# Kernel optimization log

Hardware: AMD Instinct MI355X
Metric: run time of the kernel (lower is better)

The kernel has to match this reference:

```python
import jax, jax.numpy as jnp
from jax import lax
import numpy as np

B, C, H, W = 32, 256, 56, 56
G1, G2 = 64, 4          # groups for 3x3 convs, number of parallel convs / 1x1 groups
EPS = 1e-5
DN = ('NCHW', 'OIHW', 'NCHW')


def setup_inputs() -> dict:
    key = jax.random.key(0)
    it = iter(jax.random.split(key, 32))
    nk = lambda: next(it)
    n = lambda shape, s=0.05: jax.random.normal(nk(), shape, jnp.float32) * s
    u = lambda shape: jax.random.uniform(nk(), shape, jnp.float32, minval=0.5, maxval=1.5)
    inp = {'x': jax.random.normal(nk(), (B, C, H, W), jnp.float32)}
    inp.update(
        w1=n((G2, G1, C // G1, 3, 3), 0.1), b1=n((G2, G1)),
        bn1a_g=1.0 + n((C,)), bn1a_b=n((C,)), bn1a_m=n((C,)), bn1a_v=u((C,)),
        pw1=n((C, C // G2, 1, 1), 0.1), pb1=n((C,)),
        bn1b_g=1.0 + n((C,)), bn1b_b=n((C,)), bn1b_m=n((C,)), bn1b_v=u((C,)),
        w2=n((G2, G1, C // G1, 3, 3), 0.1), b2=n((G2, G1)),
        bn2a_g=1.0 + n((C,)), bn2a_b=n((C,)), bn2a_m=n((C,)), bn2a_v=u((C,)),
        pw2=n((C, C // G2, 1, 1), 0.1), pb2=n((C,)),
        bn2b_g=1.0 + n((C,)), bn2b_b=n((C,)), bn2b_m=n((C,)), bn2b_v=u((C,)),
    )
    return inp


def _bn_relu(x, g, b, m, v):
    # inference-mode BatchNorm2d + ReLU, fused into one affine + relu
    inv = g / jnp.sqrt(v + EPS)
    return jax.nn.relu(x * inv[None, :, None, None] + (b - m * inv)[None, :, None, None])


def _gconv3x3(x, w, b):
    # Faithful to: [Conv2d(Cin, g1, k=3, p=1, groups=g1) for _ in range(g2)] then concat(dim=1).
    # Implemented as ONE grouped conv (feature_group_count=g1) followed by a cheap channel permute
    # to recover torch's concat ordering (conv-index major, group minor).
    g2, g1, cpg = w.shape[0], w.shape[1], w.shape[2]
    # combined weight: out channel k*g2 + i (group-major) uses conv i, group k
    Wc = jnp.transpose(w, (1, 0, 2, 3, 4)).reshape(g1 * g2, cpg, 3, 3)
    y = lax.conv_general_dilated(x, Wc, (1, 1), ((1, 1), (1, 1)),
                                 feature_group_count=g1, dimension_numbers=DN)
    Bx, _, Hy, Wy = y.shape
    # (g, i) ordering -> torch concat (i, g) ordering
    y = y.reshape(Bx, g1, g2, Hy, Wy).transpose(0, 2, 1, 3, 4).reshape(Bx, g1 * g2, Hy, Wy)
    return y + b.reshape(g1 * g2)[None, :, None, None]


def _pwconv(x, w, b):
    # Conv2d(C, C, k=1, groups=G2)
    y = lax.conv_general_dilated(x, w, (1, 1), 'VALID',
                                 feature_group_count=G2, dimension_numbers=DN)
    return y + b[None, :, None, None]


def reference(x, w1, b1, bn1a_g, bn1a_b, bn1a_m, bn1a_v, pw1, pb1,
              bn1b_g, bn1b_b, bn1b_m, bn1b_v,
              w2, b2, bn2a_g, bn2a_b, bn2a_m, bn2a_v, pw2, pb2,
              bn2b_g, bn2b_b, bn2b_m, bn2b_v):
    h = _gconv3x3(x, w1, b1)
    h = _bn_relu(h, bn1a_g, bn1a_b, bn1a_m, bn1a_v)
    h = _pwconv(h, pw1, pb1)
    h = _bn_relu(h, bn1b_g, bn1b_b, bn1b_m, bn1b_v)
    h = _gconv3x3(h, w2, b2)
    h = _bn_relu(h, bn2a_g, bn2a_b, bn2a_m, bn2a_v)
    h = _pwconv(h, pw2, pb2)
    h = _bn_relu(h, bn2b_g, bn2b_b, bn2b_m, bn2b_v)
    return h
```

## Files before the change

kernel.cpp:

```cpp
#include <hip/hip_runtime.h>

#define HW 3136
#define SHS 120

__global__ __launch_bounds__(256, 4) void fused_stage(
    const float* __restrict__ in,
    const float* __restrict__ gw,
    const float* __restrict__ gb,
    const float* __restrict__ bnag, const float* __restrict__ bnab,
    const float* __restrict__ bnam, const float* __restrict__ bnav,
    const float* __restrict__ pw,
    const float* __restrict__ pb,
    const float* __restrict__ bnbg, const float* __restrict__ bnbb,
    const float* __restrict__ bnbm, const float* __restrict__ bnbv,
    float* __restrict__ out)
{
    __shared__ float sH[64 * SHS];

    const int tid = threadIdx.x;

    const int idx  = blockIdx.x;
    const int xcd  = idx & 7;
    const int qq   = idx >> 3;
    const int g    = qq & 3;
    const int slot = qq >> 2;
    const int u    = slot * 8 + xcd;
    const int b    = u / 28;
    const int t    = u - b * 28;
    const int y0   = t * 2;

    const int l  = tid & 63;
    const int wv = __builtin_amdgcn_readfirstlane(tid >> 6);
    const int p  = l - 1;
    const bool pok = (unsigned)p < 56u;

    for (int kk = 0; kk < 16; ++kk) {
        const int k = wv * 16 + kk;

        float wr[36];
        {
            const float4* w4 = (const float4*)(gw + (size_t)(g * 64 + k) * 36);
#pragma unroll
            for (int j = 0; j < 9; ++j) {
                float4 v = w4[j];
                wr[4*j+0] = v.x; wr[4*j+1] = v.y; wr[4*j+2] = v.z; wr[4*j+3] = v.w;
            }
        }

        float acc0 = 0.f, acc1 = 0.f;
        const float* chp0 = in + ((size_t)(b * 256 + k * 4)) * HW;

#pragma unroll
        for (int cc = 0; cc < 4; ++cc) {
            const float* chp = chp0 + cc * HW;
            float vrow[4];
#pragma unroll
            for (int ry = 0; ry < 4; ++ry) {
                const int gy = y0 - 1 + ry;
                float v = 0.f;
                if ((unsigned)gy < 56u && pok) v = chp[gy * 56 + p];
                vrow[ry] = v;
            }
#pragma unroll
            for (int ry = 0; ry < 4; ++ry) {
                const float a  = vrow[ry];
                const float b1 = __shfl_down(a, 1);
                const float b2 = __shfl_down(a, 2);
#pragma unroll
                for (int r = 0; r < 2; ++r) {
                    const int wi = ry - r;
                    if (wi < 0 || wi > 2) continue;
                    const float w0 = wr[cc*9 + wi*3 + 0];
                    const float w1 = wr[cc*9 + wi*3 + 1];
                    const float w2 = wr[cc*9 + wi*3 + 2];
                    const float s  = fmaf(w2, b2, fmaf(w1, b1, w0 * a));
                    if (r == 0) acc0 += s; else acc1 += s;
                }
            }
        }

        const int c = g * 64 + k;
        const float sc = bnag[c] * rsqrtf(bnav[c] + 1e-5f);
        const float sh = fmaf(gb[c], sc, bnab[c] - bnam[c] * sc);
        if (l < 56) {
            sH[k * SHS + l]      = fmaxf(fmaf(acc0, sc, sh), 0.f);
            sH[k * SHS + 56 + l] = fmaxf(fmaf(acc1, sc, sh), 0.f);
        }
    }
    __syncthreads();

    const int og = tid >> 3;
    const int pg = tid & 7;

    float a2[2][14];
#pragma unroll
    for (int i = 0; i < 2; ++i)
#pragma unroll
        for (int xx = 0; xx < 14; ++xx) a2[i][xx] = 0.f;

    const float* wp0 = pw + (size_t)(g * 64 + og * 2) * 64;

    for (int c = 0; c < 64; c += 4) {
        const float4 w0 = *(const float4*)(wp0 + c);
        const float4 w1 = *(const float4*)(wp0 + 64 + c);
        const float w0a[4] = {w0.x, w0.y, w0.z, w0.w};
        const float w1a[4] = {w1.x, w1.y, w1.z, w1.w};
#pragma unroll
        for (int q2 = 0; q2 < 4; ++q2) {
            float hr[14];
#pragma unroll
            for (int j = 0; j < 7; ++j) {
                float2 v = *(const float2*)&sH[(c + q2) * SHS + 16*j + 2*pg];
                hr[2*j] = v.x; hr[2*j+1] = v.y;
            }
            const float wa = w0a[q2];
            const float wb = w1a[q2];
#pragma unroll
            for (int xx = 0; xx < 14; ++xx) {
                a2[0][xx] = fmaf(wa, hr[xx], a2[0][xx]);
                a2[1][xx] = fmaf(wb, hr[xx], a2[1][xx]);
            }
        }
    }

#pragma unroll
    for (int i = 0; i < 2; ++i) {
        const int o = g * 64 + og * 2 + i;
        const float sc = bnbg[o] * rsqrtf(bnbv[o] + 1e-5f);
        const float sh = fmaf(pb[o], sc, bnbb[o] - bnbm[o] * sc);
        float* op = out + ((size_t)(b * 256 + o)) * HW + y0 * 56;
#pragma unroll
        for (int j = 0; j < 7; ++j) {
            float v0 = fmaxf(fmaf(a2[i][2*j],   sc, sh), 0.f);
            float v1 = fmaxf(fmaf(a2[i][2*j+1], sc, sh), 0.f);
            *(float2*)(op + 16*j + 2*pg) = make_float2(v0, v1);
        }
    }
}

extern "C" void kernel_launch(void* const* d_in, const int* in_sizes, int n_in,
                              void* d_out, int out_size, void* d_ws, size_t ws_size,
                              hipStream_t stream) {
    const float* x     = (const float*)d_in[0];
    const float* w1    = (const float*)d_in[1];
    const float* b1    = (const float*)d_in[2];
    const float* bn1ag = (const float*)d_in[3];
    const float* bn1ab = (const float*)d_in[4];
    const float* bn1am = (const float*)d_in[5];
    const float* bn1av = (const float*)d_in[6];
    const float* pw1   = (const float*)d_in[7];
    const float* pb1   = (const float*)d_in[8];
    const float* bn1bg = (const float*)d_in[9];
    const float* bn1bb = (const float*)d_in[10];
    const float* bn1bm = (const float*)d_in[11];
    const float* bn1bv = (const float*)d_in[12];
    const float* w2    = (const float*)d_in[13];
    const float* b2    = (const float*)d_in[14];
    const float* bn2ag = (const float*)d_in[15];
    const float* bn2ab = (const float*)d_in[16];
    const float* bn2am = (const float*)d_in[17];
    const float* bn2av = (const float*)d_in[18];
    const float* pw2   = (const float*)d_in[19];
    const float* pb2   = (const float*)d_in[20];
    const float* bn2bg = (const float*)d_in[21];
    const float* bn2bb = (const float*)d_in[22];
    const float* bn2bm = (const float*)d_in[23];
    const float* bn2bv = (const float*)d_in[24];

    float* mid  = (float*)d_ws;
    float* outp = (float*)d_out;

    const int grid = 32 * 4 * 28;

    fused_stage<<<grid, 256, 0, stream>>>(x,   w1, b1, bn1ag, bn1ab, bn1am, bn1av,
                                          pw1, pb1, bn1bg, bn1bb, bn1bm, bn1bv, mid);
    fused_stage<<<grid, 256, 0, stream>>>(mid, w2, b2, bn2ag, bn2ab, bn2am, bn2av,
                                          pw2, pb2, bn2bg, bn2bb, bn2bm, bn2bv, outp);
}
```

Baseline: 517.1 us.

## Process four output rows per block with split-K pointwise accumulation in halves

Each block now covers four image rows instead of two, which halves the grid and reduces the 3x3 halo overhead (6 input rows read per 4 output rows instead of 4 per 2). The grouped-conv stage is split into two 32-channel halves, each staged in shared memory and consumed by the pointwise conv before the next half, so shared memory stays small. Each thread now computes 4 output channels by 14 pixels, which raises register pressure. Horizontal neighbours now come from three global loads instead of wave shuffles, and weights are read directly from global memory.

```diff
diff --git a/kernel.cpp b/kernel.cpp
--- a/kernel.cpp
+++ b/kernel.cpp
@@ -1,7 +1,7 @@
 #include <hip/hip_runtime.h>
 
 #define HW 3136
-#define SHS 120
+#define SHS4 232
 
 __global__ __launch_bounds__(256, 4) void fused_stage(
     const float* __restrict__ in,
@@ -15,7 +15,7 @@
     const float* __restrict__ bnbm, const float* __restrict__ bnbv,
     float* __restrict__ out)
 {
-    __shared__ float sH[64 * SHS];
+    __shared__ float sH[32 * SHS4];
 
     const int tid = threadIdx.x;
 
@@ -25,107 +25,105 @@
     const int g    = qq & 3;
     const int slot = qq >> 2;
     const int u    = slot * 8 + xcd;
-    const int b    = u / 28;
-    const int t    = u - b * 28;
-    const int y0   = t * 2;
+    const int b    = u / 14;
+    const int t    = u - b * 14;
+    const int y0   = t * 4;
 
     const int l  = tid & 63;
     const int wv = __builtin_amdgcn_readfirstlane(tid >> 6);
-    const int p  = l - 1;
-    const bool pok = (unsigned)p < 56u;
 
-    for (int kk = 0; kk < 16; ++kk) {
-        const int k = wv * 16 + kk;
+    const int og = tid >> 4;
+    const int pg = tid & 15;
 
-        float wr[36];
-        {
-            const float4* w4 = (const float4*)(gw + (size_t)(g * 64 + k) * 36);
+    float a2[4][14];
 #pragma unroll
-            for (int j = 0; j < 9; ++j) {
-                float4 v = w4[j];
-                wr[4*j+0] = v.x; wr[4*j+1] = v.y; wr[4*j+2] = v.z; wr[4*j+3] = v.w;
+    for (int i = 0; i < 4; ++i)
+#pragma unroll
+        for (int xx = 0; xx < 14; ++xx) a2[i][xx] = 0.f;
+
+#pragma unroll 1
+    for (int h = 0; h < 2; ++h) {
+#pragma unroll 1
+        for (int kk = 0; kk < 8; ++kk) {
+            const int k = h * 32 + wv * 8 + kk;
+            const int c = g * 64 + k;
+
+            const float* wk = gw + (size_t)(g * 64 + k) * 36;
+            float acc[4];
+#pragma unroll
+            for (int r = 0; r < 4; ++r) acc[r] = 0.f;
+
+            const float* chp0 = in + ((size_t)(b * 256 + k * 4)) * HW;
+#pragma unroll
+            for (int cc = 0; cc < 4; ++cc) {
+                const float* chp = chp0 + cc * HW;
+#pragma unroll
+                for (int ry = 0; ry < 6; ++ry) {
+                    const int gy = y0 - 1 + ry;
+                    if ((unsigned)gy >= 56u) continue;
+                    const float* rp = chp + gy * 56;
+                    const float c0 = (l >= 1 && l < 56) ? rp[l - 1] : 0.f;
+                    const float c1 = (l < 56)           ? rp[l]     : 0.f;
+                    const float c2 = (l < 55)           ? rp[l + 1] : 0.f;
+#pragma unroll
+                    for (int r = 0; r < 4; ++r) {
+                        const int wi = ry - r;
+                        if (wi < 0 || wi > 2) continue;
+                        const float w0 = wk[cc * 9 + wi * 3 + 0];
+                        const float w1 = wk[cc * 9 + wi * 3 + 1];
+                        const float w2 = wk[cc * 9 + wi * 3 + 2];
+                        acc[r] += fmaf(w2, c2, fmaf(w1, c1, w0 * c0));
+                    }
+                }
+            }
+
+            const float sc = bnag[c] * rsqrtf(bnav[c] + 1e-5f);
+            const float sh = fmaf(gb[c], sc, bnab[c] - bnam[c] * sc);
+            if (l < 56) {
+                float* sp = &sH[(k & 31) * SHS4 + l];
+                sp[0]   = fmaxf(fmaf(acc[0], sc, sh), 0.f);
+                sp[56]  = fmaxf(fmaf(acc[1], sc, sh), 0.f);
+                sp[112] = fmaxf(fmaf(acc[2], sc, sh), 0.f);
+                sp[168] = fmaxf(fmaf(acc[3], sc, sh), 0.f);
             }
         }
+        __syncthreads();
 
-        float acc0 = 0.f, acc1 = 0.f;
-        const float* chp0 = in + ((size_t)(b * 256 + k * 4)) * HW;
-
+        const float* wp = pw + (size_t)(g * 64 + og * 4) * 64 + h * 32;
+#pragma unroll 1
+        for (int c4 = 0; c4 < 32; c4 += 4) {
+            const float4 wv0 = *(const float4*)(wp + 0 * 64 + c4);
+            const float4 wv1 = *(const float4*)(wp + 1 * 64 + c4);
+            const float4 wv2 = *(const float4*)(wp + 2 * 64 + c4);
+            const float4 wv3 = *(const float4*)(wp + 3 * 64 + c4);
+            const float w0a[4] = {wv0.x, wv0.y, wv0.z, wv0.w};
+            const float w1a[4] = {wv1.x, wv1.y, wv1.z, wv1.w};
+            const float w2a[4] = {wv2.x, wv2.y, wv2.z, wv2.w};
+            const float w3a[4] = {wv3.x, wv3.y, wv3.z, wv3.w};
 #pragma unroll
-        for (int cc = 0; cc < 4; ++cc) {
-            const float* chp = chp0 + cc * HW;
-            float vrow[4];
+            for (int q2 = 0; q2 < 4; ++q2) {
+                const float* hrow = &sH[(c4 + q2) * SHS4];
+                const float wa = w0a[q2], wb = w1a[q2], wc = w2a[q2], wd = w3a[q2];
 #pragma unroll
-            for (int ry = 0; ry < 4; ++ry) {
-                const int gy = y0 - 1 + ry;
-                float v = 0.f;
-                if ((unsigned)gy < 56u && pok) v = chp[gy * 56 + p];
-                vrow[ry] = v;
-            }
-#pragma unroll
-            for (int ry = 0; ry < 4; ++ry) {
-                const float a  = vrow[ry];
-                const float b1 = __shfl_down(a, 1);
-                const float b2 = __shfl_down(a, 2);
-#pragma unroll
-                for (int r = 0; r < 2; ++r) {
-                    const int wi = ry - r;
-                    if (wi < 0 || wi > 2) continue;
-                    const float w0 = wr[cc*9 + wi*3 + 0];
-                    const float w1 = wr[cc*9 + wi*3 + 1];
-                    const float w2 = wr[cc*9 + wi*3 + 2];
-                    const float s  = fmaf(w2, b2, fmaf(w1, b1, w0 * a));
-                    if (r == 0) acc0 += s; else acc1 += s;
+                for (int j = 0; j < 7; ++j) {
+                    const float2 hv = *(const float2*)&hrow[2 * pg + 32 * j];
+                    a2[0][2*j]   = fmaf(wa, hv.x, a2[0][2*j]);
+                    a2[0][2*j+1] = fmaf(wa, hv.y, a2[0][2*j+1]);
+                    a2[1][2*j]   = fmaf(wb, hv.x, a2[1][2*j]);
+                    a2[1][2*j+1] = fmaf(wb, hv.y, a2[1][2*j+1]);
+                    a2[2][2*j]   = fmaf(wc, hv.x, a2[2][2*j]);
+                    a2[2][2*j+1] = fmaf(wc, hv.y, a2[2][2*j+1]);
+                    a2[3][2*j]   = fmaf(wd, hv.x, a2[3][2*j]);
+                    a2[3][2*j+1] = fmaf(wd, hv.y, a2[3][2*j+1]);
                 }
             }
         }
-
-        const int c = g * 64 + k;
-        const float sc = bnag[c] * rsqrtf(bnav[c] + 1e-5f);
-        const float sh = fmaf(gb[c], sc, bnab[c] - bnam[c] * sc);
-        if (l < 56) {
-            sH[k * SHS + l]      = fmaxf(fmaf(acc0, sc, sh), 0.f);
-            sH[k * SHS + 56 + l] = fmaxf(fmaf(acc1, sc, sh), 0.f);
-        }
-    }
-    __syncthreads();
-
-    const int og = tid >> 3;
-    const int pg = tid & 7;
-
-    float a2[2][14];
-#pragma unroll
-    for (int i = 0; i < 2; ++i)
-#pragma unroll
-        for (int xx = 0; xx < 14; ++xx) a2[i][xx] = 0.f;
-
-    const float* wp0 = pw + (size_t)(g * 64 + og * 2) * 64;
-
-    for (int c = 0; c < 64; c += 4) {
-        const float4 w0 = *(const float4*)(wp0 + c);
-        const float4 w1 = *(const float4*)(wp0 + 64 + c);
-        const float w0a[4] = {w0.x, w0.y, w0.z, w0.w};
-        const float w1a[4] = {w1.x, w1.y, w1.z, w1.w};
-#pragma unroll
-        for (int q2 = 0; q2 < 4; ++q2) {
-            float hr[14];
-#pragma unroll
-            for (int j = 0; j < 7; ++j) {
-                float2 v = *(const float2*)&sH[(c + q2) * SHS + 16*j + 2*pg];
-                hr[2*j] = v.x; hr[2*j+1] = v.y;
-            }
-            const float wa = w0a[q2];
-            const float wb = w1a[q2];
-#pragma unroll
-            for (int xx = 0; xx < 14; ++xx) {
-                a2[0][xx] = fmaf(wa, hr[xx], a2[0][xx]);
-                a2[1][xx] = fmaf(wb, hr[xx], a2[1][xx]);
-            }
-        }
+        __syncthreads();
     }
 
 #pragma unroll
-    for (int i = 0; i < 2; ++i) {
-        const int o = g * 64 + og * 2 + i;
+    for (int i = 0; i < 4; ++i) {
+        const int o = g * 64 + og * 4 + i;
         const float sc = bnbg[o] * rsqrtf(bnbv[o] + 1e-5f);
         const float sh = fmaf(pb[o], sc, bnbb[o] - bnbm[o] * sc);
         float* op = out + ((size_t)(b * 256 + o)) * HW + y0 * 56;
@@ -133,7 +131,7 @@
         for (int j = 0; j < 7; ++j) {
             float v0 = fmaxf(fmaf(a2[i][2*j],   sc, sh), 0.f);
             float v1 = fmaxf(fmaf(a2[i][2*j+1], sc, sh), 0.f);
-            *(float2*)(op + 16*j + 2*pg) = make_float2(v0, v1);
+            *(float2*)(op + 2 * pg + 32 * j) = make_float2(v0, v1);
         }
     }
 }
@@ -170,7 +168,7 @@
     float* mid  = (float*)d_ws;
     float* outp = (float*)d_out;
 
-    const int grid = 32 * 4 * 28;
+    const int grid = 32 * 4 * 14;
 
     fused_stage<<<grid, 256, 0, stream>>>(x,   w1, b1, bn1ag, bn1ab, bn1am, bn1av,
                                           pw1, pb1, bn1bg, bn1bb, bn1bm, bn1bv, mid);
```

New measurement: 926.1 us. 1.79x slower.

## Register-block 3x3 grouped conv over 8 pixels per lane and split into two passes

Applied to the files above, without the earlier changes.

The grouped 3x3 conv now has each lane compute 8 adjacent output pixels for two rows. It loads float4 row segments and uses only two shuffles for the halo, instead of one pixel per lane with two shuffles per row. Each wave covers 8 output channels at once, and the work is split into two passes of 32 channels. Each pass writes a half-size shared buffer that the pointwise conv consumes before the next pass. This cuts shuffle and load instruction counts and halves LDS use, which may raise occupancy. The cost is an extra barrier per block and larger register arrays.

```diff
diff --git a/kernel.cpp b/kernel.cpp
--- a/kernel.cpp
+++ b/kernel.cpp
@@ -15,7 +15,7 @@
     const float* __restrict__ bnbm, const float* __restrict__ bnbv,
     float* __restrict__ out)
 {
-    __shared__ float sH[64 * SHS];
+    __shared__ float sH[32 * SHS];
 
     const int tid = threadIdx.x;
 
@@ -30,97 +30,118 @@
     const int y0   = t * 2;
 
     const int l  = tid & 63;
-    const int wv = __builtin_amdgcn_readfirstlane(tid >> 6);
-    const int p  = l - 1;
-    const bool pok = (unsigned)p < 56u;
-
-    for (int kk = 0; kk < 16; ++kk) {
-        const int k = wv * 16 + kk;
-
-        float wr[36];
-        {
-            const float4* w4 = (const float4*)(gw + (size_t)(g * 64 + k) * 36);
-#pragma unroll
-            for (int j = 0; j < 9; ++j) {
-                float4 v = w4[j];
-                wr[4*j+0] = v.x; wr[4*j+1] = v.y; wr[4*j+2] = v.z; wr[4*j+3] = v.w;
-            }
-        }
-
-        float acc0 = 0.f, acc1 = 0.f;
+    const int wv = tid >> 6;
+    const int kq = l >> 3;
+    const int s  = l & 7;
+
+    const int og = tid >> 3;
+    const int pg = tid & 7;
+
+    float a2[2][14];
+#pragma unroll
+    for (int i = 0; i < 2; ++i)
+#pragma unroll
+        for (int xx = 0; xx < 14; ++xx) a2[i][xx] = 0.f;
+
+#pragma unroll 1
+    for (int pass = 0; pass < 2; ++pass) {
+        const int kl = wv * 8 + kq;
+        const int k  = pass * 32 + kl;
+        const int c  = g * 64 + k;
+
+        float acc[2][8];
+#pragma unroll
+        for (int r = 0; r < 2; ++r)
+#pragma unroll
+            for (int j = 0; j < 8; ++j) acc[r][j] = 0.f;
+
         const float* chp0 = in + ((size_t)(b * 256 + k * 4)) * HW;
+        const float* wkp0 = gw + (size_t)c * 36;
 
 #pragma unroll
         for (int cc = 0; cc < 4; ++cc) {
+            float wr[9];
+#pragma unroll
+            for (int j = 0; j < 9; ++j) wr[j] = wkp0[cc * 9 + j];
             const float* chp = chp0 + cc * HW;
-            float vrow[4];
 #pragma unroll
             for (int ry = 0; ry < 4; ++ry) {
                 const int gy = y0 - 1 + ry;
-                float v = 0.f;
-                if ((unsigned)gy < 56u && pok) v = chp[gy * 56 + p];
-                vrow[ry] = v;
-            }
-#pragma unroll
-            for (int ry = 0; ry < 4; ++ry) {
-                const float a  = vrow[ry];
-                const float b1 = __shfl_down(a, 1);
-                const float b2 = __shfl_down(a, 2);
+                float4 vA = make_float4(0.f, 0.f, 0.f, 0.f);
+                float4 vB = vA;
+                if ((unsigned)gy < 56u) {
+                    const float* rp = chp + gy * 56;
+                    if (s >= 1) vA = *(const float4*)(rp + 8 * s - 4);
+                    if (s <= 6) vB = *(const float4*)(rp + 8 * s);
+                }
+                const float L = __shfl_up(vB.w, 1);
+                const float R = __shfl_down(vA.x, 1);
+                const float win[10] = {L, vA.x, vA.y, vA.z, vA.w,
+                                       vB.x, vB.y, vB.z, vB.w, R};
 #pragma unroll
                 for (int r = 0; r < 2; ++r) {
                     const int wi = ry - r;
                     if (wi < 0 || wi > 2) continue;
-                    const float w0 = wr[cc*9 + wi*3 + 0];
-                    const float w1 = wr[cc*9 + wi*3 + 1];
-                    const float w2 = wr[cc*9 + wi*3 + 2];
-                    const float s  = fmaf(w2, b2, fmaf(w1, b1, w0 * a));
-                    if (r == 0) acc0 += s; else acc1 += s;
+                    const float w0 = wr[wi * 3 + 0];
+                    const float w1 = wr[wi * 3 + 1];
+                    const float w2 = wr[wi * 3 + 2];
+#pragma unroll
+                    for (int j = 0; j < 8; ++j)
+                        acc[r][j] = fmaf(w2, win[j + 2],
+                                    fmaf(w1, win[j + 1],
+                                    fmaf(w0, win[j], acc[r][j])));
                 }
             }
         }
 
-        const int c = g * 64 + k;
-        const float sc = bnag[c] * rsqrtf(bnav[c] + 1e-5f);
-        const float sh = fmaf(gb[c], sc, bnab[c] - bnam[c] * sc);
-        if (l < 56) {
-            sH[k * SHS + l]      = fmaxf(fmaf(acc0, sc, sh), 0.f);
-            sH[k * SHS + 56 + l] = fmaxf(fmaf(acc1, sc, sh), 0.f);
-        }
-    }
-    __syncthreads();
-
-    const int og = tid >> 3;
-    const int pg = tid & 7;
-
-    float a2[2][14];
-#pragma unroll
-    for (int i = 0; i < 2; ++i)
-#pragma unroll
-        for (int xx = 0; xx < 14; ++xx) a2[i][xx] = 0.f;
-
-    const float* wp0 = pw + (size_t)(g * 64 + og * 2) * 64;
-
-    for (int c = 0; c < 64; c += 4) {
-        const float4 w0 = *(const float4*)(wp0 + c);
-        const float4 w1 = *(const float4*)(wp0 + 64 + c);
-        const float w0a[4] = {w0.x, w0.y, w0.z, w0.w};
-        const float w1a[4] = {w1.x, w1.y, w1.z, w1.w};
-#pragma unroll
-        for (int q2 = 0; q2 < 4; ++q2) {
-            float hr[14];
-#pragma unroll
-            for (int j = 0; j < 7; ++j) {
-                float2 v = *(const float2*)&sH[(c + q2) * SHS + 16*j + 2*pg];
-                hr[2*j] = v.x; hr[2*j+1] = v.y;
+        {
+            const float sc = bnag[c] * rsqrtf(bnav[c] + 1e-5f);
+            const float sh = fmaf(gb[c], sc, bnab[c] - bnam[c] * sc);
+#pragma unroll
+            for (int r = 0; r < 2; ++r) {
+                float* sp = &sH[kl * SHS + r * 56];
+                if (s >= 1) {
+                    float4 v;
+                    v.x = fmaxf(fmaf(acc[r][0], sc, sh), 0.f);
+                    v.y = fmaxf(fmaf(acc[r][1], sc, sh), 0.f);
+                    v.z = fmaxf(fmaf(acc[r][2], sc, sh), 0.f);
+                    v.w = fmaxf(fmaf(acc[r][3], sc, sh), 0.f);
+                    *(float4*)(sp + 8 * s - 4) = v;
+                }
+                if (s <= 6) {
+                    float4 v;
+                    v.x = fmaxf(fmaf(acc[r][4], sc, sh), 0.f);
+                    v.y = fmaxf(fmaf(acc[r][5], sc, sh), 0.f);
+                    v.z = fmaxf(fmaf(acc[r][6], sc, sh), 0.f);
+                    v.w = fmaxf(fmaf(acc[r][7], sc, sh), 0.f);
+                    *(float4*)(sp + 8 * s) = v;
+                }
             }
-            const float wa = w0a[q2];
-            const float wb = w1a[q2];
-#pragma unroll
-            for (int xx = 0; xx < 14; ++xx) {
-                a2[0][xx] = fmaf(wa, hr[xx], a2[0][xx]);
-                a2[1][xx] = fmaf(wb, hr[xx], a2[1][xx]);
+        }
+        __syncthreads();
+
+        const float* wp = pw + (size_t)(g * 64 + og * 2) * 64 + pass * 32;
+        for (int c4 = 0; c4 < 32; c4 += 4) {
+            const float4 w0 = *(const float4*)(wp + c4);
+            const float4 w1 = *(const float4*)(wp + 64 + c4);
+            const float w0a[4] = {w0.x, w0.y, w0.z, w0.w};
+            const float w1a[4] = {w1.x, w1.y, w1.z, w1.w};
+#pragma unroll
+            for (int q2 = 0; q2 < 4; ++q2) {
+                const float* hrow = &sH[(c4 + q2) * SHS];
+                const float wa = w0a[q2];
+                const float wb = w1a[q2];
+#pragma unroll
+                for (int j = 0; j < 7; ++j) {
+                    const float2 hv = *(const float2*)&hrow[2 * pg + 16 * j];
+                    a2[0][2*j]   = fmaf(wa, hv.x, a2[0][2*j]);
+                    a2[0][2*j+1] = fmaf(wa, hv.y, a2[0][2*j+1]);
+                    a2[1][2*j]   = fmaf(wb, hv.x, a2[1][2*j]);
+                    a2[1][2*j+1] = fmaf(wb, hv.y, a2[1][2*j+1]);
+                }
             }
         }
+        if (pass == 0) __syncthreads();
     }
 
 #pragma unroll
@@ -133,7 +154,7 @@
         for (int j = 0; j < 7; ++j) {
             float v0 = fmaxf(fmaf(a2[i][2*j],   sc, sh), 0.f);
             float v1 = fmaxf(fmaf(a2[i][2*j+1], sc, sh), 0.f);
-            *(float2*)(op + 16*j + 2*pg) = make_float2(v0, v1);
+            *(float2*)(op + 2 * pg + 16 * j) = make_float2(v0, v1);
         }
     }
 }
```

After: 1.374 ms. +165.7%, slower.
